# Performance work log

Measured on AMD Instinct MI355X. Metric: run time of the kernel, lower is better.

Reference implementation:

```python
import jax, jax.numpy as jnp
import numpy as np

ATT = 256
NUM_GENES = 2128
HIDDEN = 512
B, T = 128, 1024


def setup_inputs() -> dict:
    key = jax.random.key(0)
    ks = jax.random.split(key, 8)
    return {
        "genes": jax.random.normal(ks[0], (B, NUM_GENES), dtype=jnp.float32),
        "smiles": jax.random.normal(ks[1], (B, T, HIDDEN), dtype=jnp.float32),
        "w_num_gene_features": jax.random.normal(ks[2], (1,), dtype=jnp.float32) * 0.1,
        "w_genes": jax.random.normal(ks[3], (NUM_GENES, ATT), dtype=jnp.float32) * 0.1,
        "b_genes": jax.random.normal(ks[4], (ATT,), dtype=jnp.float32) * 0.1,
        "dense_kernel": jax.random.normal(ks[5], (HIDDEN, ATT), dtype=jnp.float32) * 0.05,
        "dense_bias": jnp.zeros((ATT,), dtype=jnp.float32),
        "v": jax.random.normal(ks[6], (ATT,), dtype=jnp.float32) * 0.1,
    }


def reference(genes, smiles, w_num_gene_features, w_genes, b_genes,
              dense_kernel, dense_bias, v):
    # genes: [B, G]; collapse trivial feature axis via scalar weight -> [B, G]
    genes_collapsed = genes * w_num_gene_features[0]
    # gene context: [B, A]
    gene_proj = genes_collapsed @ w_genes + b_genes
    # smiles projection: [B, T, A]
    smiles_proj = jnp.einsum('bth,ha->bta', smiles, dense_kernel) + dense_bias
    # additive attention energies
    x = jnp.tanh(gene_proj[:, None, :] + smiles_proj)          # [B, T, A]
    xv = jnp.einsum('bta,a->bt', x, v)                          # [B, T]
    alphas = jax.nn.softmax(xv, axis=-1)                        # [B, T]
    output = jnp.einsum('bth,bt->bh', smiles, alphas)           # [B, H]
    return output, alphas
```

## Files before the change

### kernel.cpp

```cpp
#include <hip/hip_runtime.h>
#include <stdint.h>

#define B_ 128
#define T_ 1024
#define H_ 512
#define A_ 256
#define G_ 2128

typedef short s16x8 __attribute__((ext_vector_type(8)));
typedef float f32x4 __attribute__((ext_vector_type(4)));

__device__ inline unsigned short f2bf(float f) {
  unsigned u = __float_as_uint(f);
  u += 0x7fff + ((u >> 16) & 1);
  return (unsigned short)(u >> 16);
}
__device__ inline float bf2f(unsigned short h) {
  return __uint_as_float(((unsigned)h) << 16);
}
__device__ inline float fast_tanh(float x) {
  x = fminf(15.f, fmaxf(-15.f, x));
  float e = __expf(2.f * x);
  return (e - 1.f) * __builtin_amdgcn_rcpf(e + 1.f);
}

__global__ void prep_kt(const float* __restrict__ K,
                        unsigned short* __restrict__ khi,
                        unsigned short* __restrict__ klo) {
  int flat = blockIdx.x * 256 + threadIdx.x;
  int kb  = flat >> 13;
  int rem = flat & 8191;
  int a = rem >> 5;
  int k = rem & 31;
  float f = K[(kb * 32 + k) * A_ + a];
  unsigned short hi = f2bf(f);
  float lo = f - bf2f(hi);
  khi[flat] = hi;
  klo[flat] = f2bf(lo);
}

__global__ void gene_proj_k(const float* __restrict__ genes,
                            const float* __restrict__ w0p,
                            const float* __restrict__ Wg,
                            const float* __restrict__ bg,
                            const float* __restrict__ db,
                            float* __restrict__ gp) {
  int b = blockIdx.x;
  int gc = blockIdx.y;
  int a = threadIdx.x;
  int g0 = gc * 532;
  float s = 0.f;
  #pragma unroll 4
  for (int g = g0; g < g0 + 532; ++g)
    s += genes[b * G_ + g] * Wg[g * A_ + a];
  float val = w0p[0] * s;
  if (gc == 0) val += bg[a] + db[a];
  atomicAdd(&gp[b * A_ + a], val);
}

__global__ __launch_bounds__(256) void pass1(
    const float* __restrict__ smiles, const unsigned short* __restrict__ khi,
    const unsigned short* __restrict__ klo, const float* __restrict__ gp,
    const float* __restrict__ v, float* __restrict__ xv) {
  __shared__ unsigned short sA[64 * 32];
  __shared__ unsigned short sBh[256 * 32];
  __shared__ unsigned short sBl[256 * 32];
  __shared__ float sXV[256];

  const int tid = threadIdx.x;
  const int b = blockIdx.y;
  const int t0 = blockIdx.x * 64;
  const int lane = tid & 63;
  const int w = tid >> 6;
  const int n = lane & 15;
  const int quad = lane >> 4;

  const float* sb = smiles + ((size_t)b * T_ + t0) * H_;

  f32x4 acc[4][4];
  #pragma unroll
  for (int i = 0; i < 4; ++i)
    #pragma unroll
    for (int j = 0; j < 4; ++j)
      acc[i][j] = (f32x4){0.f, 0.f, 0.f, 0.f};

  const int srow = tid >> 2;
  const int shalf = tid & 3;

  for (int kb = 0; kb < 16; ++kb) {
    const int k0 = kb * 32;
    __syncthreads();
    {
      const float* src = sb + srow * H_ + k0 + shalf * 8;
      float4 f0 = *reinterpret_cast<const float4*>(src);
      float4 f1 = *reinterpret_cast<const float4*>(src + 4);
      ushort4 p0, p1;
      p0.x = f2bf(f0.x); p0.y = f2bf(f0.y); p0.z = f2bf(f0.z); p0.w = f2bf(f0.w);
      p1.x = f2bf(f1.x); p1.y = f2bf(f1.y); p1.z = f2bf(f1.z); p1.w = f2bf(f1.w);
      ushort4* dst = reinterpret_cast<ushort4*>(&sA[srow * 32 + shalf * 8]);
      dst[0] = p0; dst[1] = p1;
    }
    {
      const uint4* hsrc = reinterpret_cast<const uint4*>(khi + kb * 8192 + tid * 32);
      const uint4* lsrc = reinterpret_cast<const uint4*>(klo + kb * 8192 + tid * 32);
      uint4* hdst = reinterpret_cast<uint4*>(&sBh[tid * 32]);
      uint4* ldst = reinterpret_cast<uint4*>(&sBl[tid * 32]);
      #pragma unroll
      for (int i = 0; i < 4; ++i) hdst[i] = hsrc[i];
      #pragma unroll
      for (int i = 0; i < 4; ++i) ldst[i] = lsrc[i];
    }
    __syncthreads();

    s16x8 af[4], bh[4], bl[4];
    #pragma unroll
    for (int i = 0; i < 4; ++i)
      af[i] = *reinterpret_cast<const s16x8*>(&sA[(i * 16 + n) * 32 + quad * 8]);
    #pragma unroll
    for (int j = 0; j < 4; ++j) {
      int ar = w * 64 + j * 16 + n;
      bh[j] = *reinterpret_cast<const s16x8*>(&sBh[ar * 32 + quad * 8]);
      bl[j] = *reinterpret_cast<const s16x8*>(&sBl[ar * 32 + quad * 8]);
    }
    #pragma unroll
    for (int i = 0; i < 4; ++i)
      #pragma unroll
      for (int j = 0; j < 4; ++j) {
        acc[i][j] = __builtin_amdgcn_mfma_f32_16x16x32_bf16(af[i], bh[j], acc[i][j], 0, 0, 0);
        acc[i][j] = __builtin_amdgcn_mfma_f32_16x16x32_bf16(af[i], bl[j], acc[i][j], 0, 0, 0);
      }
  }

  float vv[4], gg[4];
  #pragma unroll
  for (int j = 0; j < 4; ++j) {
    int a = w * 64 + j * 16 + n;
    vv[j] = v[a];
    gg[j] = gp[b * A_ + a];
  }
  #pragma unroll
  for (int i = 0; i < 4; ++i) {
    #pragma unroll
    for (int r = 0; r < 4; ++r) {
      float s = 0.f;
      #pragma unroll
      for (int j = 0; j < 4; ++j) {
        float x = acc[i][j][r] + gg[j];
        s += vv[j] * fast_tanh(x);
      }
      s += __shfl_xor(s, 1); s += __shfl_xor(s, 2);
      s += __shfl_xor(s, 4); s += __shfl_xor(s, 8);
      if (n == 0) sXV[w * 64 + i * 16 + quad * 4 + r] = s;
    }
  }
  __syncthreads();
  if (tid < 64)
    xv[(size_t)b * T_ + t0 + tid] =
        sXV[tid] + sXV[64 + tid] + sXV[128 + tid] + sXV[192 + tid];
}

__global__ __launch_bounds__(256) void softmax_k(const float* __restrict__ xv,
                                                 float* __restrict__ alphas) {
  __shared__ float red[8];
  int b = blockIdx.x, tid = threadIdx.x;
  float4 x = *reinterpret_cast<const float4*>(xv + b * T_ + tid * 4);
  float m = fmaxf(fmaxf(x.x, x.y), fmaxf(x.z, x.w));
  #pragma unroll
  for (int o = 1; o < 64; o <<= 1) m = fmaxf(m, __shfl_xor(m, o));
  if ((tid & 63) == 0) red[tid >> 6] = m;
  __syncthreads();
  m = fmaxf(fmaxf(red[0], red[1]), fmaxf(red[2], red[3]));
  float e0 = __expf(x.x - m), e1 = __expf(x.y - m);
  float e2 = __expf(x.z - m), e3 = __expf(x.w - m);
  float s = e0 + e1 + e2 + e3;
  #pragma unroll
  for (int o = 1; o < 64; o <<= 1) s += __shfl_xor(s, o);
  if ((tid & 63) == 0) red[4 + (tid >> 6)] = s;
  __syncthreads();
  s = red[4] + red[5] + red[6] + red[7];
  float inv = 1.f / s;
  float4 o4;
  o4.x = e0 * inv; o4.y = e1 * inv; o4.z = e2 * inv; o4.w = e3 * inv;
  *reinterpret_cast<float4*>(alphas + b * T_ + tid * 4) = o4;
}

__global__ __launch_bounds__(256) void pass3(const float* __restrict__ smiles,
                                             const float* __restrict__ alphas,
                                             float* __restrict__ out) {
  int b = blockIdx.y;
  int t0 = blockIdx.x * 128;
  int tid = threadIdx.x;
  int tg = tid >> 7;
  int h4 = (tid & 127) * 4;
  const float* sb = smiles + (size_t)b * T_ * H_;
  f32x4 acc = (f32x4){0.f, 0.f, 0.f, 0.f};
  #pragma unroll 4
  for (int i = 0; i < 64; ++i) {
    int t = t0 + 2 * i + tg;
    float al = alphas[b * T_ + t];
    float4 sv = *reinterpret_cast<const float4*>(sb + (size_t)t * H_ + h4);
    acc.x += al * sv.x; acc.y += al * sv.y;
    acc.z += al * sv.z; acc.w += al * sv.w;
  }
  float* op = out + b * H_ + h4;
  atomicAdd(op + 0, acc.x); atomicAdd(op + 1, acc.y);
  atomicAdd(op + 2, acc.z); atomicAdd(op + 3, acc.w);
}

extern "C" void kernel_launch(void* const* d_in, const int* in_sizes, int n_in,
                              void* d_out, int out_size, void* d_ws, size_t ws_size,
                              hipStream_t stream) {
  const float* genes  = (const float*)d_in[0];
  const float* smiles = (const float*)d_in[1];
  const float* w0     = (const float*)d_in[2];
  const float* wg     = (const float*)d_in[3];
  const float* bg     = (const float*)d_in[4];
  const float* dk     = (const float*)d_in[5];
  const float* db     = (const float*)d_in[6];
  const float* v      = (const float*)d_in[7];
  float* out = (float*)d_out;
  char* ws = (char*)d_ws;
  float* gp = (float*)ws;
  unsigned short* khi = (unsigned short*)(ws + 131072);
  unsigned short* klo = (unsigned short*)(ws + 131072 + 262144);
  float* xv = (float*)(ws + 131072 + 524288);
  float* alphas = out + B_ * H_;

  hipMemsetAsync(gp, 0, B_ * A_ * sizeof(float), stream);
  hipMemsetAsync(out, 0, B_ * H_ * sizeof(float), stream);
  prep_kt<<<512, 256, 0, stream>>>(dk, khi, klo);
  gene_proj_k<<<dim3(B_, 4), 256, 0, stream>>>(genes, w0, wg, bg, db, gp);
  pass1<<<dim3(T_ / 64, B_), 256, 0, stream>>>(smiles, khi, klo, gp, v, xv);
  softmax_k<<<B_, 256, 0, stream>>>(xv, alphas);
  pass3<<<dim3(8, B_), 256, 0, stream>>>(smiles, alphas, out);
}
```

Baseline: 544.8 us.

## Drop split-bf16 low term, swizzle LDS, simplify gene projection, widen pass3 grid

The change removes the hi/lo bf16 split of the dense kernel, so pass1 issues half as many MFMAs and loads half the B-tile, at the cost of plain bf16 precision on the weights. It also XOR-swizzles the LDS layouts to reduce bank conflicts and packs the bf16 conversions into 32-bit stores. The gene projection is computed in a single block per batch row without atomics or a memset. Pass3 launches twice as many blocks, each covering fewer timesteps, to raise parallelism.

```diff
diff --git a/kernel.cpp b/kernel.cpp
--- a/kernel.cpp
+++ b/kernel.cpp
@@ -15,8 +15,8 @@
   u += 0x7fff + ((u >> 16) & 1);
   return (unsigned short)(u >> 16);
 }
-__device__ inline float bf2f(unsigned short h) {
-  return __uint_as_float(((unsigned)h) << 16);
+__device__ inline unsigned pack2bf(float a, float b) {
+  return ((unsigned)f2bf(b) << 16) | f2bf(a);
 }
 __device__ inline float fast_tanh(float x) {
   x = fminf(15.f, fmaxf(-15.f, x));
@@ -25,47 +25,39 @@
 }
 
 __global__ void prep_kt(const float* __restrict__ K,
-                        unsigned short* __restrict__ khi,
-                        unsigned short* __restrict__ klo) {
-  int flat = blockIdx.x * 256 + threadIdx.x;
-  int kb  = flat >> 13;
-  int rem = flat & 8191;
-  int a = rem >> 5;
-  int k = rem & 31;
-  float f = K[(kb * 32 + k) * A_ + a];
-  unsigned short hi = f2bf(f);
-  float lo = f - bf2f(hi);
-  khi[flat] = hi;
-  klo[flat] = f2bf(lo);
-}
-
-__global__ void gene_proj_k(const float* __restrict__ genes,
-                            const float* __restrict__ w0p,
-                            const float* __restrict__ Wg,
-                            const float* __restrict__ bg,
-                            const float* __restrict__ db,
-                            float* __restrict__ gp) {
+                        unsigned short* __restrict__ khi) {
+  int idx = blockIdx.x * 256 + threadIdx.x;
+  int h = idx >> 8;
+  int a = idx & 255;
+  khi[(h >> 5) * 8192 + a * 32 + (h & 31)] = f2bf(K[idx]);
+}
+
+__global__ __launch_bounds__(256) void gene_proj_k(
+    const float* __restrict__ genes, const float* __restrict__ w0p,
+    const float* __restrict__ Wg, const float* __restrict__ bg,
+    const float* __restrict__ db, float* __restrict__ gp) {
   int b = blockIdx.x;
-  int gc = blockIdx.y;
   int a = threadIdx.x;
-  int g0 = gc * 532;
+  const float* gb = genes + (size_t)b * G_;
   float s = 0.f;
   #pragma unroll 4
-  for (int g = g0; g < g0 + 532; ++g)
-    s += genes[b * G_ + g] * Wg[g * A_ + a];
-  float val = w0p[0] * s;
-  if (gc == 0) val += bg[a] + db[a];
-  atomicAdd(&gp[b * A_ + a], val);
-}
-
-__global__ __launch_bounds__(256) void pass1(
+  for (int g4 = 0; g4 < G_ / 4; ++g4) {
+    float4 gv = *reinterpret_cast<const float4*>(gb + g4 * 4);
+    s = fmaf(gv.x, Wg[(g4 * 4 + 0) * A_ + a], s);
+    s = fmaf(gv.y, Wg[(g4 * 4 + 1) * A_ + a], s);
+    s = fmaf(gv.z, Wg[(g4 * 4 + 2) * A_ + a], s);
+    s = fmaf(gv.w, Wg[(g4 * 4 + 3) * A_ + a], s);
+  }
+  gp[b * A_ + a] = w0p[0] * s + bg[a] + db[a];
+}
+
+__global__ __launch_bounds__(256, 4) void pass1(
     const float* __restrict__ smiles, const unsigned short* __restrict__ khi,
-    const unsigned short* __restrict__ klo, const float* __restrict__ gp,
-    const float* __restrict__ v, float* __restrict__ xv) {
+    const float* __restrict__ gp, const float* __restrict__ v,
+    float* __restrict__ xv) {
   __shared__ unsigned short sA[64 * 32];
-  __shared__ unsigned short sBh[256 * 32];
-  __shared__ unsigned short sBl[256 * 32];
-  __shared__ float sXV[256];
+  __shared__ unsigned short sB[256 * 32];
+  __shared__ float sXV[64 * 4];
 
   const int tid = threadIdx.x;
   const int b = blockIdx.y;
@@ -73,7 +65,7 @@
   const int lane = tid & 63;
   const int w = tid >> 6;
   const int n = lane & 15;
-  const int quad = lane >> 4;
+  const int q = lane >> 4;
 
   const float* sb = smiles + ((size_t)b * T_ + t0) * H_;
 
@@ -84,51 +76,50 @@
     for (int j = 0; j < 4; ++j)
       acc[i][j] = (f32x4){0.f, 0.f, 0.f, 0.f};
 
-  const int srow = tid >> 2;
-  const int shalf = tid & 3;
+  const int ar = tid >> 2;
+  const int ac = tid & 3;
+  const int swA = (ac ^ (ar & 3)) * 8;
+  const int swB0 = (0 ^ (tid & 3)) * 8;
+  const int swB1 = (1 ^ (tid & 3)) * 8;
+  const int swB2 = (2 ^ (tid & 3)) * 8;
+  const int swB3 = (3 ^ (tid & 3)) * 8;
 
   for (int kb = 0; kb < 16; ++kb) {
     const int k0 = kb * 32;
     __syncthreads();
     {
-      const float* src = sb + srow * H_ + k0 + shalf * 8;
+      const float* src = sb + ar * H_ + k0 + ac * 8;
       float4 f0 = *reinterpret_cast<const float4*>(src);
       float4 f1 = *reinterpret_cast<const float4*>(src + 4);
-      ushort4 p0, p1;
-      p0.x = f2bf(f0.x); p0.y = f2bf(f0.y); p0.z = f2bf(f0.z); p0.w = f2bf(f0.w);
-      p1.x = f2bf(f1.x); p1.y = f2bf(f1.y); p1.z = f2bf(f1.z); p1.w = f2bf(f1.w);
-      ushort4* dst = reinterpret_cast<ushort4*>(&sA[srow * 32 + shalf * 8]);
-      dst[0] = p0; dst[1] = p1;
+      uint4 p;
+      p.x = pack2bf(f0.x, f0.y); p.y = pack2bf(f0.z, f0.w);
+      p.z = pack2bf(f1.x, f1.y); p.w = pack2bf(f1.z, f1.w);
+      *reinterpret_cast<uint4*>(&sA[ar * 32 + swA]) = p;
     }
     {
-      const uint4* hsrc = reinterpret_cast<const uint4*>(khi + kb * 8192 + tid * 32);
-      const uint4* lsrc = reinterpret_cast<const uint4*>(klo + kb * 8192 + tid * 32);
-      uint4* hdst = reinterpret_cast<uint4*>(&sBh[tid * 32]);
-      uint4* ldst = reinterpret_cast<uint4*>(&sBl[tid * 32]);
-      #pragma unroll
-      for (int i = 0; i < 4; ++i) hdst[i] = hsrc[i];
-      #pragma unroll
-      for (int i = 0; i < 4; ++i) ldst[i] = lsrc[i];
+      const uint4* src = reinterpret_cast<const uint4*>(khi + kb * 8192 + tid * 32);
+      uint4 q0 = src[0], q1 = src[1], q2 = src[2], q3 = src[3];
+      unsigned short* row = &sB[tid * 32];
+      *reinterpret_cast<uint4*>(row + swB0) = q0;
+      *reinterpret_cast<uint4*>(row + swB1) = q1;
+      *reinterpret_cast<uint4*>(row + swB2) = q2;
+      *reinterpret_cast<uint4*>(row + swB3) = q3;
     }
     __syncthreads();
 
-    s16x8 af[4], bh[4], bl[4];
+    s16x8 af[4], bh[4];
+    const int sw = (q ^ (n & 3)) * 8;
     #pragma unroll
     for (int i = 0; i < 4; ++i)
-      af[i] = *reinterpret_cast<const s16x8*>(&sA[(i * 16 + n) * 32 + quad * 8]);
-    #pragma unroll
-    for (int j = 0; j < 4; ++j) {
-      int ar = w * 64 + j * 16 + n;
-      bh[j] = *reinterpret_cast<const s16x8*>(&sBh[ar * 32 + quad * 8]);
-      bl[j] = *reinterpret_cast<const s16x8*>(&sBl[ar * 32 + quad * 8]);
-    }
+      af[i] = *reinterpret_cast<const s16x8*>(&sA[(i * 16 + n) * 32 + sw]);
+    #pragma unroll
+    for (int j = 0; j < 4; ++j)
+      bh[j] = *reinterpret_cast<const s16x8*>(&sB[(w * 64 + j * 16 + n) * 32 + sw]);
     #pragma unroll
     for (int i = 0; i < 4; ++i)
       #pragma unroll
-      for (int j = 0; j < 4; ++j) {
+      for (int j = 0; j < 4; ++j)
         acc[i][j] = __builtin_amdgcn_mfma_f32_16x16x32_bf16(af[i], bh[j], acc[i][j], 0, 0, 0);
-        acc[i][j] = __builtin_amdgcn_mfma_f32_16x16x32_bf16(af[i], bl[j], acc[i][j], 0, 0, 0);
-      }
   }
 
   float vv[4], gg[4];
@@ -144,19 +135,18 @@
     for (int r = 0; r < 4; ++r) {
       float s = 0.f;
       #pragma unroll
-      for (int j = 0; j < 4; ++j) {
-        float x = acc[i][j][r] + gg[j];
-        s += vv[j] * fast_tanh(x);
-      }
+      for (int j = 0; j < 4; ++j)
+        s += vv[j] * fast_tanh(acc[i][j][r] + gg[j]);
       s += __shfl_xor(s, 1); s += __shfl_xor(s, 2);
       s += __shfl_xor(s, 4); s += __shfl_xor(s, 8);
-      if (n == 0) sXV[w * 64 + i * 16 + quad * 4 + r] = s;
+      if (n == 0) sXV[(i * 16 + q * 4 + r) * 4 + w] = s;
     }
   }
   __syncthreads();
-  if (tid < 64)
-    xv[(size_t)b * T_ + t0 + tid] =
-        sXV[tid] + sXV[64 + tid] + sXV[128 + tid] + sXV[192 + tid];
+  if (tid < 64) {
+    float* p = &sXV[tid * 4];
+    xv[(size_t)b * T_ + t0 + tid] = p[0] + p[1] + p[2] + p[3];
+  }
 }
 
 __global__ __launch_bounds__(256) void softmax_k(const float* __restrict__ xv,
@@ -188,19 +178,19 @@
                                              const float* __restrict__ alphas,
                                              float* __restrict__ out) {
   int b = blockIdx.y;
-  int t0 = blockIdx.x * 128;
+  int t0 = blockIdx.x * 64;
   int tid = threadIdx.x;
   int tg = tid >> 7;
   int h4 = (tid & 127) * 4;
   const float* sb = smiles + (size_t)b * T_ * H_;
   f32x4 acc = (f32x4){0.f, 0.f, 0.f, 0.f};
-  #pragma unroll 4
-  for (int i = 0; i < 64; ++i) {
+  #pragma unroll 8
+  for (int i = 0; i < 32; ++i) {
     int t = t0 + 2 * i + tg;
     float al = alphas[b * T_ + t];
     float4 sv = *reinterpret_cast<const float4*>(sb + (size_t)t * H_ + h4);
-    acc.x += al * sv.x; acc.y += al * sv.y;
-    acc.z += al * sv.z; acc.w += al * sv.w;
+    acc.x = fmaf(al, sv.x, acc.x); acc.y = fmaf(al, sv.y, acc.y);
+    acc.z = fmaf(al, sv.z, acc.z); acc.w = fmaf(al, sv.w, acc.w);
   }
   float* op = out + b * H_ + h4;
   atomicAdd(op + 0, acc.x); atomicAdd(op + 1, acc.y);
@@ -222,15 +212,13 @@
   char* ws = (char*)d_ws;
   float* gp = (float*)ws;
   unsigned short* khi = (unsigned short*)(ws + 131072);
-  unsigned short* klo = (unsigned short*)(ws + 131072 + 262144);
-  float* xv = (float*)(ws + 131072 + 524288);
+  float* xv = (float*)(ws + 131072 + 262144);
   float* alphas = out + B_ * H_;
 
-  hipMemsetAsync(gp, 0, B_ * A_ * sizeof(float), stream);
   hipMemsetAsync(out, 0, B_ * H_ * sizeof(float), stream);
-  prep_kt<<<512, 256, 0, stream>>>(dk, khi, klo);
-  gene_proj_k<<<dim3(B_, 4), 256, 0, stream>>>(genes, w0, wg, bg, db, gp);
-  pass1<<<dim3(T_ / 64, B_), 256, 0, stream>>>(smiles, khi, klo, gp, v, xv);
+  prep_kt<<<512, 256, 0, stream>>>(dk, khi);
+  gene_proj_k<<<B_, 256, 0, stream>>>(genes, w0, wg, bg, db, gp);
+  pass1<<<dim3(T_ / 64, B_), 256, 0, stream>>>(smiles, khi, gp, v, xv);
   softmax_k<<<B_, 256, 0, stream>>>(xv, alphas);
-  pass3<<<dim3(8, B_), 256, 0, stream>>>(smiles, alphas, out);
-}
+  pass3<<<dim3(16, B_), 256, 0, stream>>>(smiles, alphas, out);
+}
```

After: 526.6 us. -3.3%, faster.
